# Kernel optimization log

Measured on AMD Instinct MI355X. Metric: run time of the kernel, lower is better.

The kernel has to match this reference:

```python
import jax, jax.numpy as jnp
import numpy as np

N_NODES = 50000
N_EDGES = 800000
NDIM_IN = 128
EDIM_IN = 128
NDIM_OUT = 128
EDIM_OUT = 128


def setup_inputs() -> dict:
    key = jax.random.key(0)
    ks = jax.random.split(key, 8)
    nfeats = jax.random.normal(ks[0], (N_NODES, NDIM_IN), dtype=jnp.float32)
    efeats = jax.random.normal(ks[1], (N_EDGES, EDIM_IN), dtype=jnp.float32)
    u = jax.random.randint(ks[2], (N_EDGES,), 0, N_NODES, dtype=jnp.int32)
    v = jax.random.randint(ks[3], (N_EDGES,), 0, N_NODES, dtype=jnp.int32)
    # torch.nn.Linear params: weight [out, in], bias [out]
    d_apply_in = 2 * NDIM_IN + EDIM_IN  # concat(nfeats, h_neigh)
    lim1 = 1.0 / np.sqrt(d_apply_in)
    W_apply_w = jax.random.uniform(ks[4], (NDIM_OUT, d_apply_in), jnp.float32, -lim1, lim1)
    W_apply_b = jax.random.uniform(ks[5], (NDIM_OUT,), jnp.float32, -lim1, lim1)
    lim2 = 1.0 / np.sqrt(2 * NDIM_OUT)
    W_edge_w = jax.random.uniform(ks[6], (EDIM_OUT, 2 * NDIM_OUT), jnp.float32, -lim2, lim2)
    W_edge_b = jax.random.uniform(ks[7], (EDIM_OUT,), jnp.float32, -lim2, lim2)
    return {"nfeats": nfeats, "efeats": efeats, "u": u, "v": v,
            "W_apply_w": W_apply_w, "W_apply_b": W_apply_b,
            "W_edge_w": W_edge_w, "W_edge_b": W_edge_b}


def reference(nfeats, efeats, u, v, W_apply_w, W_apply_b, W_edge_w, W_edge_b):
    n_nodes = nfeats.shape[0]
    # message per edge: concat(src node h, edge h)  -> [E, ndim_in+edim_in]
    msg = jnp.concatenate([nfeats[u], efeats], axis=1)
    # mean reduction over incoming edges at dst node v (0 for isolated nodes, like DGL)
    sums = jax.ops.segment_sum(msg, v, num_segments=n_nodes)
    counts = jax.ops.segment_sum(jnp.ones((msg.shape[0],), msg.dtype), v, num_segments=n_nodes)
    h_neigh = jnp.where(counts[:, None] > 0, sums / jnp.maximum(counts, 1.0)[:, None], 0.0)
    # node update
    h_nodes_new = jnp.concatenate([nfeats, h_neigh], axis=1) @ W_apply_w.T + W_apply_b
    h_nodes_new = jax.nn.relu(h_nodes_new)
    # edge update
    edge_input = jnp.concatenate([h_nodes_new[u], h_nodes_new[v]], axis=1)
    h_edges_new = jax.nn.relu(edge_input @ W_edge_w.T + W_edge_b)
    return h_nodes_new, h_edges_new
```

## Files before the change

### kernel.cpp

```cpp
#include <hip/hip_runtime.h>
#include <hip/hip_bf16.h>

#define N_NODES_C 50000
#define N_EDGES_C 800000
#define NBLK_NODES 196
#define EDGE_HEAD_ROWS 50048

typedef __attribute__((ext_vector_type(8))) short bf16x8;
typedef __attribute__((ext_vector_type(4))) float f32x4;

__device__ __forceinline__ unsigned short f2bf(float f) {
    unsigned int x = __float_as_uint(f);
    unsigned int r = x + 0x7fffu + ((x >> 16) & 1u);
    return (unsigned short)(r >> 16);
}
__device__ __forceinline__ float bf2f(unsigned short s) {
    return __uint_as_float(((unsigned int)s) << 16);
}

__global__ __launch_bounds__(256) void zero_k(int* __restrict__ cnt)
{
    int i = blockIdx.x * 256 + threadIdx.x;
    if (i < N_NODES_C) cnt[i] = 0;
}

__global__ __launch_bounds__(256) void count_k(const int* __restrict__ v, int* __restrict__ cnt)
{
    int e = blockIdx.x * 256 + threadIdx.x;
    atomicAdd(&cnt[v[e]], 1);
}

__global__ __launch_bounds__(256) void scan_partial_k(
    const int* __restrict__ cnt, int* __restrict__ bsum)
{
    __shared__ int ws[4];
    int b = blockIdx.x, t = threadIdx.x, lane = t & 63, wid = t >> 6;
    int i = b * 256 + t;
    int x = (i < N_NODES_C) ? cnt[i] : 0;
    int s = x;
#pragma unroll
    for (int d = 1; d < 64; d <<= 1) {
        int tv = __shfl_up(s, d, 64);
        if (lane >= d) s += tv;
    }
    if (lane == 63) ws[wid] = s;
    __syncthreads();
    if (t == 0) bsum[b] = ws[0] + ws[1] + ws[2] + ws[3];
}

__global__ __launch_bounds__(256) void scan_block_k(
    const int* __restrict__ bsum, int* __restrict__ boff, int* __restrict__ rowst)
{
    __shared__ int ws[4];
    int t = threadIdx.x, lane = t & 63, wid = t >> 6;
    int x = (t < NBLK_NODES) ? bsum[t] : 0;
    int s = x;
#pragma unroll
    for (int d = 1; d < 64; d <<= 1) {
        int tv = __shfl_up(s, d, 64);
        if (lane >= d) s += tv;
    }
    if (lane == 63) ws[wid] = s;
    __syncthreads();
    if (t == 0) {
        int a = 0;
#pragma unroll
        for (int w = 0; w < 4; ++w) { int tmp = ws[w]; ws[w] = a; a += tmp; }
    }
    __syncthreads();
    int excl = ws[wid] + s - x;
    if (t < NBLK_NODES) boff[t] = excl;
    if (t == 255) rowst[N_NODES_C] = excl;
}

__global__ __launch_bounds__(256) void scan_scatter_k(
    const int* __restrict__ cnt, const int* __restrict__ boff,
    int* __restrict__ rowst, int* __restrict__ cursor)
{
    __shared__ int ws[4];
    int b = blockIdx.x, t = threadIdx.x, lane = t & 63, wid = t >> 6;
    int i = b * 256 + t;
    int x = (i < N_NODES_C) ? cnt[i] : 0;
    int s = x;
#pragma unroll
    for (int d = 1; d < 64; d <<= 1) {
        int tv = __shfl_up(s, d, 64);
        if (lane >= d) s += tv;
    }
    if (lane == 63) ws[wid] = s;
    __syncthreads();
    if (t == 0) {
        int a = 0;
#pragma unroll
        for (int w = 0; w < 4; ++w) { int tmp = ws[w]; ws[w] = a; a += tmp; }
    }
    __syncthreads();
    int excl = boff[b] + ws[wid] + s - x;
    if (i < N_NODES_C) { rowst[i] = excl; cursor[i] = excl; }
}

__global__ __launch_bounds__(256) void fill_k(const int* __restrict__ v,
                                              const int* __restrict__ u,
                                              int* __restrict__ cursor,
                                              int2* __restrict__ pairs)
{
    int e = blockIdx.x * 256 + threadIdx.x;
    int pos = atomicAdd(&cursor[v[e]], 1);
    pairs[pos] = make_int2(e, u[e]);
}

__global__ __launch_bounds__(256) void aggregate_k(
    const int2* __restrict__ pairs, const int* __restrict__ rowst,
    const float* __restrict__ nfeats, const float* __restrict__ efeats,
    unsigned short* __restrict__ hnb)
{
    int wv   = blockIdx.x * 4 + (threadIdx.x >> 6);
    int lane = threadIdx.x & 63;
    if (wv >= N_NODES_C) return;
    int s = rowst[wv], e_end = rowst[wv + 1];
    int deg = e_end - s;

    float4 a0 = make_float4(0.f, 0.f, 0.f, 0.f);
    float4 a1 = a0, a2 = a0, a3 = a0;
    int i = s;
    for (; i + 3 < e_end; i += 4) {
        int2 p0 = pairs[i + 0];
        int2 p1 = pairs[i + 1];
        int2 p2 = pairs[i + 2];
        int2 p3 = pairs[i + 3];
        const float* s0 = (lane < 32) ? (nfeats + (size_t)p0.y * 128 + lane * 4)
                                      : (efeats + (size_t)p0.x * 128 + (lane - 32) * 4);
        const float* s1 = (lane < 32) ? (nfeats + (size_t)p1.y * 128 + lane * 4)
                                      : (efeats + (size_t)p1.x * 128 + (lane - 32) * 4);
        const float* s2 = (lane < 32) ? (nfeats + (size_t)p2.y * 128 + lane * 4)
                                      : (efeats + (size_t)p2.x * 128 + (lane - 32) * 4);
        const float* s3 = (lane < 32) ? (nfeats + (size_t)p3.y * 128 + lane * 4)
                                      : (efeats + (size_t)p3.x * 128 + (lane - 32) * 4);
        float4 v0 = *reinterpret_cast<const float4*>(s0);
        float4 v1 = *reinterpret_cast<const float4*>(s1);
        float4 v2 = *reinterpret_cast<const float4*>(s2);
        float4 v3 = *reinterpret_cast<const float4*>(s3);
        a0.x += v0.x; a0.y += v0.y; a0.z += v0.z; a0.w += v0.w;
        a1.x += v1.x; a1.y += v1.y; a1.z += v1.z; a1.w += v1.w;
        a2.x += v2.x; a2.y += v2.y; a2.z += v2.z; a2.w += v2.w;
        a3.x += v3.x; a3.y += v3.y; a3.z += v3.z; a3.w += v3.w;
    }
    for (; i < e_end; ++i) {
        int2 p = pairs[i];
        const float* src = (lane < 32) ? (nfeats + (size_t)p.y * 128 + lane * 4)
                                       : (efeats + (size_t)p.x * 128 + (lane - 32) * 4);
        float4 vv = *reinterpret_cast<const float4*>(src);
        a0.x += vv.x; a0.y += vv.y; a0.z += vv.z; a0.w += vv.w;
    }
    a0.x += a1.x + a2.x + a3.x;
    a0.y += a1.y + a2.y + a3.y;
    a0.z += a1.z + a2.z + a3.z;
    a0.w += a1.w + a2.w + a3.w;
    float r = (deg > 0) ? 1.f / (float)deg : 0.f;
    ushort4 o;
    o.x = f2bf(a0.x * r); o.y = f2bf(a0.y * r);
    o.z = f2bf(a0.z * r); o.w = f2bf(a0.w * r);
    *reinterpret_cast<ushort4*>(hnb + (size_t)wv * 256 + lane * 4) = o;
}

__device__ __forceinline__ void stage_half_row(
    const float* __restrict__ src, char* __restrict__ lds, int row, int halfg)
{
#pragma unroll
    for (int g = 0; g < 4; ++g) {
        float4 f0 = reinterpret_cast<const float4*>(src)[g * 2 + 0];
        float4 f1 = reinterpret_cast<const float4*>(src)[g * 2 + 1];
        union { unsigned short s[8]; uint4 q; } pk;
        pk.s[0] = f2bf(f0.x); pk.s[1] = f2bf(f0.y);
        pk.s[2] = f2bf(f0.z); pk.s[3] = f2bf(f0.w);
        pk.s[4] = f2bf(f1.x); pk.s[5] = f2bf(f1.y);
        pk.s[6] = f2bf(f1.z); pk.s[7] = f2bf(f1.w);
        int byteoff = ((halfg * 4 + g) * 16) ^ ((row & 7) << 4);
        *reinterpret_cast<uint4*>(lds + row * 128 + byteoff) = pk.q;
    }
}

__device__ __forceinline__ void stage_half_row_cp(
    const unsigned short* __restrict__ src, char* __restrict__ lds, int row, int halfg)
{
#pragma unroll
    for (int g = 0; g < 4; ++g) {
        uint4 q = reinterpret_cast<const uint4*>(src)[g];
        int byteoff = ((halfg * 4 + g) * 16) ^ ((row & 7) << 4);
        *reinterpret_cast<uint4*>(lds + row * 128 + byteoff) = q;
    }
}

__device__ __forceinline__ void mfma_slab(
    const char* __restrict__ Xs, const char* __restrict__ Ws,
    int wm, int wn, int lane, f32x4 (&acc)[4][4])
{
#pragma unroll
    for (int c = 0; c < 2; ++c) {
        int kb = c * 64 + (lane >> 4) * 16;
        bf16x8 a[4], b[4];
#pragma unroll
        for (int i = 0; i < 4; ++i) {
            int row = wm * 64 + i * 16 + (lane & 15);
            a[i] = *reinterpret_cast<const bf16x8*>(
                Xs + row * 128 + (kb ^ ((row & 7) << 4)));
        }
#pragma unroll
        for (int j = 0; j < 4; ++j) {
            int row = wn * 64 + j * 16 + (lane & 15);
            b[j] = *reinterpret_cast<const bf16x8*>(
                Ws + row * 128 + (kb ^ ((row & 7) << 4)));
        }
#pragma unroll
        for (int i = 0; i < 4; ++i)
#pragma unroll
            for (int j = 0; j < 4; ++j)
                acc[i][j] = __builtin_amdgcn_mfma_f32_16x16x32_bf16(
                    a[i], b[j], acc[i][j], 0, 0, 0);
    }
}

__device__ __forceinline__ void epilogue_store(
    const f32x4 (&acc)[4][4], const float* __restrict__ bias,
    float* __restrict__ out, int row_base, int row_limit, int wm, int wn, int lane)
{
    int col0 = wn * 64 + (lane & 15);
    int row0 = row_base + wm * 64 + (lane >> 4) * 4;
#pragma unroll
    for (int j = 0; j < 4; ++j) {
        float bj = bias[col0 + j * 16];
#pragma unroll
        for (int i = 0; i < 4; ++i) {
#pragma unroll
            for (int r = 0; r < 4; ++r) {
                int row = row0 + i * 16 + r;
                if (row < row_limit) {
                    float val = fmaxf(acc[i][j][r] + bj, 0.f);
                    out[(size_t)row * 128 + col0 + j * 16] = val;
                }
            }
        }
    }
}

__global__ __launch_bounds__(256) void prep_w_k(
    const float* __restrict__ Wa, const float* __restrict__ We,
    unsigned short* __restrict__ wa, unsigned short* __restrict__ we)
{
    int i = blockIdx.x * 256 + threadIdx.x;
    if (i < 49152)      wa[i] = f2bf(Wa[i]);
    else if (i < 81920) we[i - 49152] = f2bf(We[i - 49152]);
}

__global__ __launch_bounds__(256) void node_k(
    const float* __restrict__ nfeats, const unsigned short* __restrict__ hnb,
    const unsigned short* __restrict__ wa, const float* __restrict__ bias,
    float* __restrict__ out)
{
    __shared__ uint4 XsBuf[1024];
    __shared__ uint4 WsBuf[1024];
    char* Xs = (char*)XsBuf;
    char* Ws = (char*)WsBuf;

    int tid = threadIdx.x;
    int n0  = blockIdx.x * 128;
    int wave = tid >> 6, lane = tid & 63;
    int wm = wave >> 1, wn = wave & 1;
    int srow = tid >> 1, shalf = tid & 1;

    int nrow = n0 + srow;
    if (nrow >= N_NODES_C) nrow = N_NODES_C - 1;

    f32x4 acc[4][4];
#pragma unroll
    for (int i = 0; i < 4; ++i)
#pragma unroll
        for (int j = 0; j < 4; ++j) acc[i][j] = (f32x4)0.f;

#pragma unroll
    for (int k0 = 0; k0 < 384; k0 += 64) {
        if (k0 < 128)
            stage_half_row(nfeats + (size_t)nrow * 128 + k0 + shalf * 32,
                           Xs, srow, shalf);
        else
            stage_half_row_cp(hnb + (size_t)nrow * 256 + (k0 - 128) + shalf * 32,
                              Xs, srow, shalf);
        stage_half_row_cp(wa + (size_t)srow * 384 + k0 + shalf * 32,
                          Ws, srow, shalf);
        __syncthreads();
        mfma_slab(Xs, Ws, wm, wn, lane, acc);
        __syncthreads();
    }

    epilogue_store(acc, bias, out, n0, N_NODES_C, wm, wn, lane);
}

__global__ __launch_bounds__(256) void pp_k(
    const float* __restrict__ h, const unsigned short* __restrict__ we,
    unsigned short* __restrict__ P)
{
    __shared__ uint4 XsBuf[1024];
    __shared__ uint4 WsBuf[1024];
    char* Xs = (char*)XsBuf;
    char* Ws = (char*)WsBuf;

    int tid = threadIdx.x;
    int n0  = blockIdx.x * 128;
    int cb  = blockIdx.y;
    int wave = tid >> 6, lane = tid & 63;
    int wm = wave >> 1, wn = wave & 1;
    int srow = tid >> 1, shalf = tid & 1;

    int nrow = n0 + srow;
    if (nrow >= N_NODES_C) nrow = N_NODES_C - 1;

    f32x4 acc[4][4];
#pragma unroll
    for (int i = 0; i < 4; ++i)
#pragma unroll
        for (int j = 0; j < 4; ++j) acc[i][j] = (f32x4)0.f;

#pragma unroll
    for (int k0 = 0; k0 < 128; k0 += 64) {
        stage_half_row(h + (size_t)nrow * 128 + k0 + shalf * 32, Xs, srow, shalf);
        stage_half_row_cp(we + (size_t)srow * 256 + cb * 128 + k0 + shalf * 32,
                          Ws, srow, shalf);
        __syncthreads();
        mfma_slab(Xs, Ws, wm, wn, lane, acc);
        __syncthreads();
    }

    int col0 = wn * 64 + (lane & 15);
    int row0 = n0 + wm * 64 + (lane >> 4) * 4;
#pragma unroll
    for (int j = 0; j < 4; ++j) {
#pragma unroll
        for (int i = 0; i < 4; ++i) {
#pragma unroll
            for (int r = 0; r < 4; ++r) {
                int row = row0 + i * 16 + r;
                if (row < N_NODES_C)
                    P[(size_t)row * 256 + cb * 128 + col0 + j * 16] = f2bf(acc[i][j][r]);
            }
        }
    }
}

__global__ __launch_bounds__(256) void edge_add_k(
    const unsigned short* __restrict__ P, const int* __restrict__ u,
    const int* __restrict__ v, const float* __restrict__ bias,
    float* __restrict__ out, int e_base)
{
    int c = blockIdx.x * 256 + threadIdx.x;
    int e = e_base + (c >> 5);
    int q = c & 31;
    int uu = u[e], vv = v[e];
    ushort4 pa = *reinterpret_cast<const ushort4*>(P + (size_t)uu * 256 + q * 4);
    ushort4 pb = *reinterpret_cast<const ushort4*>(P + (size_t)vv * 256 + 128 + q * 4);
    float4 b4 = *reinterpret_cast<const float4*>(bias + q * 4);
    float4 o;
    o.x = fmaxf(bf2f(pa.x) + bf2f(pb.x) + b4.x, 0.f);
    o.y = fmaxf(bf2f(pa.y) + bf2f(pb.y) + b4.y, 0.f);
    o.z = fmaxf(bf2f(pa.z) + bf2f(pb.z) + b4.z, 0.f);
    o.w = fmaxf(bf2f(pa.w) + bf2f(pb.w) + b4.w, 0.f);
    *reinterpret_cast<float4*>(out + (size_t)e * 128 + q * 4) = o;
}

__global__ __launch_bounds__(256) void edge_head_k(
    const float* __restrict__ h, const int* __restrict__ u,
    const int* __restrict__ v, const float* __restrict__ W,
    const float* __restrict__ bias, float* __restrict__ out)
{
    __shared__ uint4 XsBuf[1024];
    __shared__ uint4 WsBuf[1024];
    __shared__ int us[128], vs[128];
    char* Xs = (char*)XsBuf;
    char* Ws = (char*)WsBuf;

    int tid = threadIdx.x;
    int e0  = blockIdx.x * 128;
    if (tid < 128) us[tid]       = u[e0 + tid];
    else           vs[tid - 128] = v[e0 + tid - 128];
    __syncthreads();

    int wave = tid >> 6, lane = tid & 63;
    int wm = wave >> 1, wn = wave & 1;
    int srow = tid >> 1, shalf = tid & 1;

    f32x4 acc[4][4];
#pragma unroll
    for (int i = 0; i < 4; ++i)
#pragma unroll
        for (int j = 0; j < 4; ++j) acc[i][j] = (f32x4)0.f;

#pragma unroll
    for (int k0 = 0; k0 < 256; k0 += 64) {
        int node = (k0 < 128) ? us[srow] : vs[srow];
        stage_half_row(h + (size_t)node * 128 + (k0 & 127) + shalf * 32,
                       Xs, srow, shalf);
        stage_half_row(W + (size_t)srow * 256 + k0 + shalf * 32,
                       Ws, srow, shalf);
        __syncthreads();
        mfma_slab(Xs, Ws, wm, wn, lane, acc);
        __syncthreads();
    }

    epilogue_store(acc, bias, out, e0, N_EDGES_C, wm, wn, lane);
}

extern "C" void kernel_launch(void* const* d_in, const int* in_sizes, int n_in,
                              void* d_out, int out_size, void* d_ws, size_t ws_size,
                              hipStream_t stream)
{
    const float* nfeats    = (const float*)d_in[0];
    const float* efeats    = (const float*)d_in[1];
    const int*   u         = (const int*)d_in[2];
    const int*   v         = (const int*)d_in[3];
    const float* W_apply_w = (const float*)d_in[4];
    const float* W_apply_b = (const float*)d_in[5];
    const float* W_edge_w  = (const float*)d_in[6];
    const float* W_edge_b  = (const float*)d_in[7];

    float* out      = (float*)d_out;
    float* h_nodes  = out;
    float* edge_out = out + (size_t)N_NODES_C * 128;

    unsigned short* hnb = (unsigned short*)edge_out;
    int*   cnt     = (int*)(edge_out + 6400000);
    int*   rowst   = cnt + N_NODES_C;
    int*   cursor  = rowst + N_NODES_C + 1;
    int2*  pairs   = (int2*)(cursor + N_NODES_C + 2);
    int*   bsum    = (int*)(pairs + N_EDGES_C);
    int*   boff    = bsum + 256;
    unsigned short* wa = (unsigned short*)(boff + 256);
    unsigned short* we = wa + 49152;

    const size_t P_ELEMS = (size_t)N_NODES_C * 256;
    bool p_in_ws = ws_size >= P_ELEMS * sizeof(unsigned short);
    unsigned short* P = p_in_ws ? (unsigned short*)d_ws
                                : (unsigned short*)edge_out;

    zero_k<<<NBLK_NODES, 256, 0, stream>>>(cnt);
    prep_w_k<<<320, 256, 0, stream>>>(W_apply_w, W_edge_w, wa, we);
    count_k<<<N_EDGES_C / 256, 256, 0, stream>>>(v, cnt);
    scan_partial_k<<<NBLK_NODES, 256, 0, stream>>>(cnt, bsum);
    scan_block_k<<<1, 256, 0, stream>>>(bsum, boff, rowst);
    scan_scatter_k<<<NBLK_NODES, 256, 0, stream>>>(cnt, boff, rowst, cursor);
    fill_k<<<N_EDGES_C / 256, 256, 0, stream>>>(v, u, cursor, pairs);
    aggregate_k<<<N_NODES_C / 4, 256, 0, stream>>>(pairs, rowst, nfeats, efeats, hnb);

    node_k<<<(N_NODES_C + 127) / 128, 256, 0, stream>>>(
        nfeats, hnb, wa, W_apply_b, h_nodes);

    pp_k<<<dim3((N_NODES_C + 127) / 128, 2), 256, 0, stream>>>(
        h_nodes, we, P);

    if (p_in_ws) {
        edge_add_k<<<N_EDGES_C * 32 / 256, 256, 0, stream>>>(
            P, u, v, W_edge_b, edge_out, 0);
    } else {
        edge_add_k<<<(N_EDGES_C - EDGE_HEAD_ROWS) * 32 / 256, 256, 0, stream>>>(
            P, u, v, W_edge_b, edge_out, EDGE_HEAD_ROWS);
        edge_head_k<<<EDGE_HEAD_ROWS / 128, 256, 0, stream>>>(
            h_nodes, u, v, W_edge_w, W_edge_b, edge_out);
    }
}
```

Baseline: 415.4 us.

## Fuse node projection into node kernel, merge setup kernels, widen aggregate gather

Merges the zero-count and weight-conversion kernels into one setup launch, and folds the per-node edge projection (P = h_nodes @ We halves) into the node kernel so each block reprojects its own freshly written h rows. The aggregation loop now batches eight edge gathers with clamped indices and exits early for zero-degree nodes, aiming for more memory-level parallelism. The fused node kernel reads back its own global output after a block barrier, relying on intra-block visibility of those writes, and it runs a longer serial chain per block with fewer total blocks.

Result: no change. 409.2 us (-1.5%).

```diff
diff --git a/kernel.cpp b/kernel.cpp
--- a/kernel.cpp
+++ b/kernel.cpp
@@ -18,10 +18,22 @@
     return __uint_as_float(((unsigned int)s) << 16);
 }
 
-__global__ __launch_bounds__(256) void zero_k(int* __restrict__ cnt)
-{
-    int i = blockIdx.x * 256 + threadIdx.x;
-    if (i < N_NODES_C) cnt[i] = 0;
+__global__ __launch_bounds__(256) void setup_k(
+    const float* __restrict__ Wa, const float* __restrict__ We,
+    unsigned short* __restrict__ wa, unsigned short* __restrict__ we,
+    int* __restrict__ cnt)
+{
+    int b = blockIdx.x, t = threadIdx.x;
+    if (b < 196) {
+        int i = b * 256 + t;
+        if (i < N_NODES_C) cnt[i] = 0;
+    } else if (b < 388) {
+        int i = (b - 196) * 256 + t;
+        wa[i] = f2bf(Wa[i]);
+    } else {
+        int i = (b - 388) * 256 + t;
+        we[i] = f2bf(We[i]);
+    }
 }
 
 __global__ __launch_bounds__(256) void count_k(const int* __restrict__ v, int* __restrict__ cnt)
@@ -120,43 +132,44 @@
     int s = rowst[wv], e_end = rowst[wv + 1];
     int deg = e_end - s;
 
+    if (deg == 0) {
+        *reinterpret_cast<ushort4*>(hnb + (size_t)wv * 256 + lane * 4) =
+            make_ushort4(0, 0, 0, 0);
+        return;
+    }
+
     float4 a0 = make_float4(0.f, 0.f, 0.f, 0.f);
     float4 a1 = a0, a2 = a0, a3 = a0;
-    int i = s;
-    for (; i + 3 < e_end; i += 4) {
-        int2 p0 = pairs[i + 0];
-        int2 p1 = pairs[i + 1];
-        int2 p2 = pairs[i + 2];
-        int2 p3 = pairs[i + 3];
-        const float* s0 = (lane < 32) ? (nfeats + (size_t)p0.y * 128 + lane * 4)
-                                      : (efeats + (size_t)p0.x * 128 + (lane - 32) * 4);
-        const float* s1 = (lane < 32) ? (nfeats + (size_t)p1.y * 128 + lane * 4)
-                                      : (efeats + (size_t)p1.x * 128 + (lane - 32) * 4);
-        const float* s2 = (lane < 32) ? (nfeats + (size_t)p2.y * 128 + lane * 4)
-                                      : (efeats + (size_t)p2.x * 128 + (lane - 32) * 4);
-        const float* s3 = (lane < 32) ? (nfeats + (size_t)p3.y * 128 + lane * 4)
-                                      : (efeats + (size_t)p3.x * 128 + (lane - 32) * 4);
-        float4 v0 = *reinterpret_cast<const float4*>(s0);
-        float4 v1 = *reinterpret_cast<const float4*>(s1);
-        float4 v2 = *reinterpret_cast<const float4*>(s2);
-        float4 v3 = *reinterpret_cast<const float4*>(s3);
-        a0.x += v0.x; a0.y += v0.y; a0.z += v0.z; a0.w += v0.w;
-        a1.x += v1.x; a1.y += v1.y; a1.z += v1.z; a1.w += v1.w;
-        a2.x += v2.x; a2.y += v2.y; a2.z += v2.z; a2.w += v2.w;
-        a3.x += v3.x; a3.y += v3.y; a3.z += v3.z; a3.w += v3.w;
-    }
-    for (; i < e_end; ++i) {
-        int2 p = pairs[i];
-        const float* src = (lane < 32) ? (nfeats + (size_t)p.y * 128 + lane * 4)
-                                       : (efeats + (size_t)p.x * 128 + (lane - 32) * 4);
-        float4 vv = *reinterpret_cast<const float4*>(src);
-        a0.x += vv.x; a0.y += vv.y; a0.z += vv.z; a0.w += vv.w;
+    for (int base = s; base < e_end; base += 8) {
+        int2 p[8];
+#pragma unroll
+        for (int t = 0; t < 8; ++t) {
+            int idx = base + t;
+            p[t] = pairs[idx < e_end ? idx : e_end - 1];
+        }
+        float4 val[8];
+#pragma unroll
+        for (int t = 0; t < 8; ++t) {
+            const float* src = (lane < 32)
+                ? (nfeats + (size_t)p[t].y * 128 + lane * 4)
+                : (efeats + (size_t)p[t].x * 128 + (lane - 32) * 4);
+            val[t] = *reinterpret_cast<const float4*>(src);
+        }
+#pragma unroll
+        for (int t = 0; t < 8; ++t) {
+            if (base + t < e_end) {
+                float4* a = (t & 2) ? ((t & 1) ? &a3 : &a2)
+                                    : ((t & 1) ? &a1 : &a0);
+                a->x += val[t].x; a->y += val[t].y;
+                a->z += val[t].z; a->w += val[t].w;
+            }
+        }
     }
     a0.x += a1.x + a2.x + a3.x;
     a0.y += a1.y + a2.y + a3.y;
     a0.z += a1.z + a2.z + a3.z;
     a0.w += a1.w + a2.w + a3.w;
-    float r = (deg > 0) ? 1.f / (float)deg : 0.f;
+    float r = 1.f / (float)deg;
     ushort4 o;
     o.x = f2bf(a0.x * r); o.y = f2bf(a0.y * r);
     o.z = f2bf(a0.z * r); o.w = f2bf(a0.w * r);
@@ -243,19 +256,11 @@
     }
 }
 
-__global__ __launch_bounds__(256) void prep_w_k(
-    const float* __restrict__ Wa, const float* __restrict__ We,
-    unsigned short* __restrict__ wa, unsigned short* __restrict__ we)
-{
-    int i = blockIdx.x * 256 + threadIdx.x;
-    if (i < 49152)      wa[i] = f2bf(Wa[i]);
-    else if (i < 81920) we[i - 49152] = f2bf(We[i - 49152]);
-}
-
 __global__ __launch_bounds__(256) void node_k(
     const float* __restrict__ nfeats, const unsigned short* __restrict__ hnb,
-    const unsigned short* __restrict__ wa, const float* __restrict__ bias,
-    float* __restrict__ out)
+    const unsigned short* __restrict__ wa, const unsigned short* __restrict__ we,
+    const float* __restrict__ bias, float* __restrict__ out,
+    unsigned short* __restrict__ P)
 {
     __shared__ uint4 XsBuf[1024];
     __shared__ uint4 WsBuf[1024];
@@ -293,54 +298,41 @@
     }
 
     epilogue_store(acc, bias, out, n0, N_NODES_C, wm, wn, lane);
-}
-
-__global__ __launch_bounds__(256) void pp_k(
-    const float* __restrict__ h, const unsigned short* __restrict__ we,
-    unsigned short* __restrict__ P)
-{
-    __shared__ uint4 XsBuf[1024];
-    __shared__ uint4 WsBuf[1024];
-    char* Xs = (char*)XsBuf;
-    char* Ws = (char*)WsBuf;
-
-    int tid = threadIdx.x;
-    int n0  = blockIdx.x * 128;
-    int cb  = blockIdx.y;
-    int wave = tid >> 6, lane = tid & 63;
-    int wm = wave >> 1, wn = wave & 1;
-    int srow = tid >> 1, shalf = tid & 1;
-
-    int nrow = n0 + srow;
-    if (nrow >= N_NODES_C) nrow = N_NODES_C - 1;
-
-    f32x4 acc[4][4];
-#pragma unroll
-    for (int i = 0; i < 4; ++i)
-#pragma unroll
-        for (int j = 0; j < 4; ++j) acc[i][j] = (f32x4)0.f;
-
-#pragma unroll
-    for (int k0 = 0; k0 < 128; k0 += 64) {
-        stage_half_row(h + (size_t)nrow * 128 + k0 + shalf * 32, Xs, srow, shalf);
-        stage_half_row_cp(we + (size_t)srow * 256 + cb * 128 + k0 + shalf * 32,
-                          Ws, srow, shalf);
-        __syncthreads();
-        mfma_slab(Xs, Ws, wm, wn, lane, acc);
-        __syncthreads();
-    }
+    __syncthreads();
 
     int col0 = wn * 64 + (lane & 15);
     int row0 = n0 + wm * 64 + (lane >> 4) * 4;
 #pragma unroll
-    for (int j = 0; j < 4; ++j) {
-#pragma unroll
-        for (int i = 0; i < 4; ++i) {
-#pragma unroll
-            for (int r = 0; r < 4; ++r) {
-                int row = row0 + i * 16 + r;
-                if (row < N_NODES_C)
-                    P[(size_t)row * 256 + cb * 128 + col0 + j * 16] = f2bf(acc[i][j][r]);
+    for (int cb = 0; cb < 2; ++cb) {
+        f32x4 accP[4][4];
+#pragma unroll
+        for (int i = 0; i < 4; ++i)
+#pragma unroll
+            for (int j = 0; j < 4; ++j) accP[i][j] = (f32x4)0.f;
+
+#pragma unroll
+        for (int s2 = 0; s2 < 2; ++s2) {
+            int k0 = s2 * 64;
+            stage_half_row(out + (size_t)nrow * 128 + k0 + shalf * 32,
+                           Xs, srow, shalf);
+            stage_half_row_cp(we + (size_t)srow * 256 + cb * 128 + k0 + shalf * 32,
+                              Ws, srow, shalf);
+            __syncthreads();
+            mfma_slab(Xs, Ws, wm, wn, lane, accP);
+            __syncthreads();
+        }
+
+#pragma unroll
+        for (int j = 0; j < 4; ++j) {
+#pragma unroll
+            for (int i = 0; i < 4; ++i) {
+#pragma unroll
+                for (int r = 0; r < 4; ++r) {
+                    int row = row0 + i * 16 + r;
+                    if (row < N_NODES_C)
+                        P[(size_t)row * 256 + cb * 128 + col0 + j * 16] =
+                            f2bf(accP[i][j][r]);
+                }
             }
         }
     }
@@ -440,8 +432,7 @@
     unsigned short* P = p_in_ws ? (unsigned short*)d_ws
                                 : (unsigned short*)edge_out;
 
-    zero_k<<<NBLK_NODES, 256, 0, stream>>>(cnt);
-    prep_w_k<<<320, 256, 0, stream>>>(W_apply_w, W_edge_w, wa, we);
+    setup_k<<<516, 256, 0, stream>>>(W_apply_w, W_edge_w, wa, we, cnt);
     count_k<<<N_EDGES_C / 256, 256, 0, stream>>>(v, cnt);
     scan_partial_k<<<NBLK_NODES, 256, 0, stream>>>(cnt, bsum);
     scan_block_k<<<1, 256, 0, stream>>>(bsum, boff, rowst);
@@ -450,10 +441,7 @@
     aggregate_k<<<N_NODES_C / 4, 256, 0, stream>>>(pairs, rowst, nfeats, efeats, hnb);
 
     node_k<<<(N_NODES_C + 127) / 128, 256, 0, stream>>>(
-        nfeats, hnb, wa, W_apply_b, h_nodes);
-
-    pp_k<<<dim3((N_NODES_C + 127) / 128, 2), 256, 0, stream>>>(
-        h_nodes, we, P);
+        nfeats, hnb, wa, we, W_apply_b, h_nodes, P);
 
     if (p_in_ws) {
         edge_add_k<<<N_EDGES_C * 32 / 256, 256, 0, stream>>>(
```
